# Kernel tuning notes

Measured on AMD Instinct MI355X. Metric: run time of the kernel, lower is better.

The kernel has to match this reference:

```python
import jax, jax.numpy as jnp
import numpy as np

N, E, G = 50000, 800000, 64
IN, ED = 2, 2
H1, C1 = 16, 8
H2, C2 = 4, 16
D1 = H1 * C1  # 128
D2 = H2 * C2  # 64


def _glorot(key, shape):
    fan_in, fan_out = shape[0], shape[-1]
    lim = jnp.sqrt(6.0 / (fan_in + fan_out))
    return jax.random.uniform(key, shape, jnp.float32, -lim, lim)


def setup_inputs() -> dict:
    key = jax.random.key(0)
    ks = jax.random.split(key, 16)
    x = jax.random.normal(ks[0], (N, IN), jnp.float32)
    edge_attr = jax.random.uniform(ks[1], (E, ED), jnp.float32)
    edge_index = jax.random.randint(ks[2], (2, E), 0, N, jnp.int64)
    batch = jnp.sort(jax.random.randint(ks[3], (N,), 0, G, jnp.int64))
    return {
        'x': x, 'edge_attr': edge_attr,
        'W_l1': _glorot(ks[4], (IN, D1)), 'b_l1': jnp.zeros((D1,), jnp.float32),
        'W_r1': _glorot(ks[5], (IN, D1)), 'b_r1': jnp.zeros((D1,), jnp.float32),
        'W_e1': _glorot(ks[6], (ED, D1)),
        'att1': _glorot(ks[7], (H1, C1)),
        'bias1': jnp.zeros((D1,), jnp.float32),
        'W_l2': _glorot(ks[8], (D1, D2)), 'b_l2': jnp.zeros((D2,), jnp.float32),
        'W_r2': _glorot(ks[9], (D1, D2)), 'b_r2': jnp.zeros((D2,), jnp.float32),
        'W_e2': _glorot(ks[10], (ED, D2)),
        'att2': _glorot(ks[11], (H2, C2)),
        'bias2': jnp.zeros((D2,), jnp.float32),
        'edge_index': edge_index, 'batch': batch,
    }


def _gatv2(x, edge_attr, src, tgt, Wl, bl, Wr, br, We, att, bias, H, C):
    n = x.shape[0]
    xl = (x @ Wl + bl).reshape(n, H, C)          # source transform (lin_l)
    xr = (x @ Wr + br).reshape(n, H, C)          # target transform (lin_r)
    xe = (edge_attr @ We).reshape(-1, H, C)      # edge transform (no bias)
    m = xl[src] + xr[tgt] + xe                   # [E,H,C]
    e = jnp.einsum('ehc,hc->eh', jax.nn.leaky_relu(m, 0.2), att)  # [E,H]
    emax = jax.ops.segment_max(e, tgt, num_segments=n)
    ee = jnp.exp(e - emax[tgt])
    denom = jax.ops.segment_sum(ee, tgt, num_segments=n)
    alpha = ee / denom[tgt]                      # segment softmax over in-edges
    out = jax.ops.segment_sum(alpha[:, :, None] * xl[src], tgt, num_segments=n)
    return out.reshape(n, H * C) + bias


def reference(x, edge_attr, W_l1, b_l1, W_r1, b_r1, W_e1, att1, bias1,
              W_l2, b_l2, W_r2, b_r2, W_e2, att2, bias2, edge_index, batch):
    src, tgt = edge_index[0], edge_index[1]
    h = _gatv2(x, edge_attr, src, tgt, W_l1, b_l1, W_r1, b_r1, W_e1, att1, bias1, H1, C1)
    h = jax.nn.elu(h)  # dropout is identity in eval mode
    h = _gatv2(h, edge_attr, src, tgt, W_l2, b_l2, W_r2, b_r2, W_e2, att2, bias2, H2, C2)
    # global_mean_pool over graphs
    sums = jax.ops.segment_sum(h, batch, num_segments=G)
    cnts = jax.ops.segment_sum(jnp.ones((h.shape[0], 1), h.dtype), batch, num_segments=G)
    return sums / jnp.maximum(cnts, 1.0)
```

## Files before the change

### kernel.cpp

```cpp
#include <hip/hip_runtime.h>
#include <math.h>

#define NBLK 256


template<int CTRL>
__device__ __forceinline__ float dppf(float x) {
    return __int_as_float(__builtin_amdgcn_update_dpp(
        0, __float_as_int(x), CTRL, 0xF, 0xF, true));
}
__device__ __forceinline__ float quadsum(float x) {
    x += dppf<0xB1>(x);
    x += dppf<0x4E>(x);
    return x;
}
__device__ __forceinline__ float sum16(float x) {
    x += dppf<0xB1>(x);
    x += dppf<0x4E>(x);
    x += dppf<0x141>(x);
    x += dppf<0x140>(x);
    return x;
}


__global__ __launch_bounds__(256) void k_hist(const int* __restrict__ tgt,
                                              int* __restrict__ gh,
                                              int e, int chunk, int nbuck) {
    __shared__ int lh[256];
    int tid = threadIdx.x, blk = blockIdx.x;
    lh[tid] = 0;
    __syncthreads();
    int lo = blk * chunk, hi = min(lo + chunk, e);
    for (int i = lo + tid; i < hi; i += 256)
        atomicAdd(&lh[tgt[i] >> 8], 1);
    __syncthreads();
    if (tid < nbuck) gh[tid * NBLK + blk] = lh[tid];
}


__global__ __launch_bounds__(256) void k_scanA(const int* __restrict__ deg,
                                               int* __restrict__ excl,
                                               int* __restrict__ bsum, int n) {
    int i = blockIdx.x * 256 + threadIdx.x;
    int lane = threadIdx.x & 63, wv = threadIdx.x >> 6;
    int v = (i < n) ? deg[i] : 0;
    int incl = v;
#pragma unroll
    for (int off = 1; off < 64; off <<= 1) {
        int t = __shfl_up(incl, off);
        if (lane >= off) incl += t;
    }
    __shared__ int ws[4];
    if (lane == 63) ws[wv] = incl;
    __syncthreads();
    int prefix = 0;
    for (int k = 0; k < wv; ++k) prefix += ws[k];
    if (i < n) excl[i] = prefix + incl - v;
    if (threadIdx.x == 255) bsum[blockIdx.x] = prefix + incl;
}

__global__ __launch_bounds__(256) void k_scanB(const int* __restrict__ bsum, int* __restrict__ boff,
                                               int* __restrict__ total_at, int nb, int n) {
    __shared__ int ws[4];
    __shared__ int carry_s;
    int lane = threadIdx.x & 63, wv = threadIdx.x >> 6;
    if (threadIdx.x == 0) carry_s = 0;
    __syncthreads();
    for (int base = 0; base < nb; base += 256) {
        int i = base + threadIdx.x;
        int v = (i < nb) ? bsum[i] : 0;
        int incl = v;
#pragma unroll
        for (int off = 1; off < 64; off <<= 1) {
            int t = __shfl_up(incl, off);
            if (lane >= off) incl += t;
        }
        if (lane == 63) ws[wv] = incl;
        __syncthreads();
        int prefix = carry_s;
        for (int k = 0; k < wv; ++k) prefix += ws[k];
        if (i < nb) boff[i] = prefix + incl - v;
        __syncthreads();
        if (threadIdx.x == 255) carry_s = prefix + incl;
        __syncthreads();
    }
    if (threadIdx.x == 0) total_at[n] = carry_s;
}

__global__ void k_scanC(int* __restrict__ arr, const int* __restrict__ boff, int n) {
    int i = blockIdx.x * 256 + threadIdx.x;
    if (i < n) arr[i] += boff[blockIdx.x];
}


__global__ __launch_bounds__(256) void k_binplace(const int* __restrict__ src,
                                                  const int* __restrict__ tgt,
                                                  const float* __restrict__ ea,
                                                  const float* __restrict__ x,
                                                  const int* __restrict__ gexcl,
                                                  float4* __restrict__ brec,
                                                  int* __restrict__ bmeta,
                                                  int e, int chunk, int nbuck) {
    __shared__ int loff[256];
    int tid = threadIdx.x, blk = blockIdx.x;
    if (tid < nbuck) loff[tid] = gexcl[tid * NBLK + blk];
    __syncthreads();
    int lo = blk * chunk, hi = min(lo + chunk, e);
    for (int i = lo + tid; i < hi; i += 256) {
        int t = tgt[i], s = src[i];
        float2 ev = ((const float2*)ea)[i];
        float2 xv = *(const float2*)(x + 2 * (size_t)s);
        int dst = atomicAdd(&loff[t >> 8], 1);
        brec[dst] = make_float4(xv.x, xv.y, ev.x, ev.y);
        bmeta[dst] = (s & 0xFFFF) | ((t & 0xFF) << 16);
    }
}


__global__ __launch_bounds__(256) void k_place2(const int* __restrict__ gexcl,
                                                const int* __restrict__ bmeta,
                                                const float4* __restrict__ brec,
                                                float4* __restrict__ col_rec,
                                                int* __restrict__ col_src,
                                                int* __restrict__ rowp, int n) {
    __shared__ int hist[256];
    __shared__ int pos[256];
    __shared__ int ws[4];
    int b = blockIdx.x, tid = threadIdx.x;
    int lo = gexcl[b * NBLK], hi = gexcl[(b + 1) * NBLK];
    hist[tid] = 0;
    __syncthreads();
    for (int i = lo + tid; i < hi; i += 256)
        atomicAdd(&hist[(bmeta[i] >> 16) & 0xFF], 1);
    __syncthreads();
    int lane = tid & 63, wv = tid >> 6;
    int v = hist[tid];
    int incl = v;
#pragma unroll
    for (int off = 1; off < 64; off <<= 1) {
        int t = __shfl_up(incl, off);
        if (lane >= off) incl += t;
    }
    if (lane == 63) ws[wv] = incl;
    __syncthreads();
    int prefix = 0;
    for (int k = 0; k < wv; ++k) prefix += ws[k];
    int rp = lo + prefix + incl - v;
    int node = b * 256 + tid;
    if (node <= n) rowp[node] = rp;
    if (b == (int)gridDim.x - 1 && tid == 0) rowp[n] = hi;
    pos[tid] = rp;
    __syncthreads();
    for (int i = lo + tid; i < hi; i += 256) {
        int m = bmeta[i];
        float4 r = brec[i];
        int slot = atomicAdd(&pos[(m >> 16) & 0xFF], 1);
        col_rec[slot] = r;
        col_src[slot] = m & 0xFFFF;
    }
}


__global__ __launch_bounds__(256) void k_agg1(
    const float* __restrict__ x,
    const int* __restrict__ rowp,
    const float4* __restrict__ col_rec,
    const float* __restrict__ W_l1, const float* __restrict__ b_l1,
    const float* __restrict__ W_r1, const float* __restrict__ b_r1,
    const float* __restrict__ W_e1,
    const float* __restrict__ att1,
    const float* __restrict__ bias1,
    float* __restrict__ hpost,
    int n)
{
    int wid = (blockIdx.x * blockDim.x + threadIdx.x) >> 6;
    if (wid >= n) return;
    int v = __builtin_amdgcn_readfirstlane(wid);
    int lane = threadIdx.x & 63;
    int f0 = 2 * lane, f1 = 2 * lane + 1;

    float Wl00 = W_l1[f0], Wl10 = W_l1[128 + f0], bl0 = b_l1[f0];
    float Wl01 = W_l1[f1], Wl11 = W_l1[128 + f1], bl1 = b_l1[f1];
    float We00 = W_e1[f0], We10 = W_e1[128 + f0];
    float We01 = W_e1[f1], We11 = W_e1[128 + f1];
    float a0 = att1[f0], a1 = att1[f1];

    float xv0 = x[2 * v], xv1 = x[2 * v + 1];
    float xrA = xv0 * W_r1[f0] + xv1 * W_r1[128 + f0] + b_r1[f0];
    float xrB = xv0 * W_r1[f1] + xv1 * W_r1[128 + f1] + b_r1[f1];

    float lh = 0.f, acc0 = 0.f, acc1 = 0.f;
    int rs = rowp[v], re = rowp[v + 1];
    bool b0 = (lane & 1) != 0, b1 = (lane & 2) != 0;

    int cs = rs;
#define E1(K, R) \
    float xa##K = fmaf(R.x, Wl00, fmaf(R.y, Wl10, bl0)); \
    float xb##K = fmaf(R.x, Wl01, fmaf(R.y, Wl11, bl1)); \
    float s##K; { \
        float m0 = xa##K + xrA + R.z * We00 + R.w * We10; \
        float m1 = xb##K + xrB + R.z * We01 + R.w * We11; \
        s##K = quadsum(fmaf(fmaxf(m0, 0.2f * m0), a0, fmaxf(m1, 0.2f * m1) * a1)); \
    }
    for (; cs + 4 <= re; cs += 4) {
        float4 r0 = col_rec[cs + 0];
        float4 r1 = col_rec[cs + 1];
        float4 r2 = col_rec[cs + 2];
        float4 r3 = col_rec[cs + 3];
        E1(0, r0) E1(1, r1) E1(2, r2) E1(3, r3)
        float sel01 = b0 ? s1 : s0;
        float sel23 = b0 ? s3 : s2;
        float smy = b1 ? sel23 : sel01;
        float p = __expf(smy);
        float p0 = dppf<0x00>(p), p1 = dppf<0x55>(p), p2 = dppf<0xAA>(p), p3 = dppf<0xFF>(p);
        lh += (p0 + p1) + (p2 + p3);
        acc0 += fmaf(p0, xa0, p1 * xa1) + fmaf(p2, xa2, p3 * xa3);
        acc1 += fmaf(p0, xb0, p1 * xb1) + fmaf(p2, xb2, p3 * xb3);
    }
#undef E1
    for (; cs < re; ++cs) {
        float4 r = col_rec[cs];
        float xa = fmaf(r.x, Wl00, fmaf(r.y, Wl10, bl0));
        float xb = fmaf(r.x, Wl01, fmaf(r.y, Wl11, bl1));
        float m0 = xa + xrA + r.z * We00 + r.w * We10;
        float m1 = xb + xrB + r.z * We01 + r.w * We11;
        float s = quadsum(fmaf(fmaxf(m0, 0.2f * m0), a0, fmaxf(m1, 0.2f * m1) * a1));
        float p = __expf(s);
        lh += p;
        acc0 = fmaf(p, xa, acc0);
        acc1 = fmaf(p, xb, acc1);
    }

    float r0o, r1o;
    if (re > rs) { float inv = 1.f / lh; r0o = acc0 * inv; r1o = acc1 * inv; }
    else { r0o = 0.f; r1o = 0.f; }
    r0o += bias1[f0]; r1o += bias1[f1];
    r0o = (r0o > 0.f) ? r0o : (__expf(r0o) - 1.f);
    r1o = (r1o > 0.f) ? r1o : (__expf(r1o) - 1.f);
    *(float2*)(hpost + (size_t)v * 128 + f0) = make_float2(r0o, r1o);
}


struct XF2Shared {
    float4 hs[64 * 32];
    float4 ws[128 * 16];
};

__device__ __forceinline__ void xf2_pass(XF2Shared& sm,
                                         const float* __restrict__ W,
                                         const float* __restrict__ b,
                                         float* __restrict__ out,
                                         int v0, int n, int t) {
    __syncthreads();
    {
        const float4* wsrc = (const float4*)W;
#pragma unroll
        for (int i = 0; i < 8; ++i) sm.ws[t + 256 * i] = wsrc[t + 256 * i];
    }
    __syncthreads();

    int lane = t & 63, w = t >> 6;
    int fg = lane & 3, ng = lane >> 2;
    int fq = 4 * w + fg;
    int hsw = ng & 7;

    float acc[4][4];
#pragma unroll
    for (int i = 0; i < 4; ++i)
#pragma unroll
        for (int c = 0; c < 4; ++c) acc[i][c] = 0.f;

    for (int kq = 0; kq < 32; ++kq) {
        float4 w0 = sm.ws[(4 * kq + 0) * 16 + fq];
        float4 w1 = sm.ws[(4 * kq + 1) * 16 + fq];
        float4 w2 = sm.ws[(4 * kq + 2) * 16 + fq];
        float4 w3 = sm.ws[(4 * kq + 3) * 16 + fq];
        int ks = kq ^ hsw;
        float4 h0 = sm.hs[(4 * ng + 0) * 32 + ks];
        float4 h1 = sm.hs[(4 * ng + 1) * 32 + ks];
        float4 h2 = sm.hs[(4 * ng + 2) * 32 + ks];
        float4 h3 = sm.hs[(4 * ng + 3) * 32 + ks];
#pragma unroll
        for (int i = 0; i < 4; ++i) {
            float4 h = (i == 0) ? h0 : (i == 1) ? h1 : (i == 2) ? h2 : h3;
            acc[i][0] += h.x * w0.x; acc[i][1] += h.x * w0.y; acc[i][2] += h.x * w0.z; acc[i][3] += h.x * w0.w;
            acc[i][0] += h.y * w1.x; acc[i][1] += h.y * w1.y; acc[i][2] += h.y * w1.z; acc[i][3] += h.y * w1.w;
            acc[i][0] += h.z * w2.x; acc[i][1] += h.z * w2.y; acc[i][2] += h.z * w2.z; acc[i][3] += h.z * w2.w;
            acc[i][0] += h.w * w3.x; acc[i][1] += h.w * w3.y; acc[i][2] += h.w * w3.z; acc[i][3] += h.w * w3.w;
        }
    }

    float4 bf = ((const float4*)b)[fq];
#pragma unroll
    for (int i = 0; i < 4; ++i) {
        int node = v0 + 4 * ng + i;
        if (node < n) {
            float4 r = make_float4(acc[i][0] + bf.x, acc[i][1] + bf.y,
                                   acc[i][2] + bf.z, acc[i][3] + bf.w);
            *(float4*)(out + (size_t)node * 64 + 4 * fq) = r;
        }
    }
}

__global__ __launch_bounds__(256) void k_transform2(
    const float* __restrict__ hpost,
    const float* __restrict__ W_l2, const float* __restrict__ b_l2,
    const float* __restrict__ W_r2, const float* __restrict__ b_r2,
    float* __restrict__ xl2, float* __restrict__ xr2, int n)
{
    __shared__ XF2Shared sm;
    int t = threadIdx.x;
    int v0 = blockIdx.x * 64;
    {
        int node = t >> 2, sub = t & 3;
        int sw = (node >> 2) & 7;
        bool valid = (v0 + node) < n;
        const float4* src = (const float4*)(hpost + (size_t)(v0 + node) * 128);
#pragma unroll
        for (int i = 0; i < 8; ++i) {
            int kq = sub + 4 * i;
            float4 val = valid ? src[kq] : make_float4(0.f, 0.f, 0.f, 0.f);
            sm.hs[node * 32 + (kq ^ sw)] = val;
        }
    }
    xf2_pass(sm, W_l2, b_l2, xl2, v0, n, t);
    xf2_pass(sm, W_r2, b_r2, xr2, v0, n, t);
}


__global__ __launch_bounds__(256) void k_agg2(
    const float* __restrict__ xl2,
    const float* __restrict__ xr2,
    const int* __restrict__ rowp,
    const int* __restrict__ col_src,
    const float4* __restrict__ col_rec,
    const float* __restrict__ W_e2,
    const float* __restrict__ att2,
    const float* __restrict__ bias2,
    float* __restrict__ h2,
    int n)
{
    int wid = (blockIdx.x * blockDim.x + threadIdx.x) >> 6;
    if (wid >= n) return;
    int v = __builtin_amdgcn_readfirstlane(wid);
    int lane = threadIdx.x & 63;
    float We0 = W_e2[lane], We1 = W_e2[64 + lane];
    float a = att2[lane];
    float xr = xr2[(size_t)v * 64 + lane];
    float lh = 0.f, acc = 0.f;
    int rs = rowp[v], re = rowp[v + 1];
    const float2* eap = (const float2*)col_rec;
    bool b0 = (lane & 1) != 0, b1 = (lane & 2) != 0;

    int cs = rs;
#define E2(K, EV, XL) \
    float s##K; { \
        float m = XL + xr + EV.x * We0 + EV.y * We1; \
        s##K = sum16(fmaxf(m, 0.2f * m) * a); \
    }
    for (; cs + 4 <= re; cs += 4) {
        int u0 = col_src[cs], u1 = col_src[cs + 1], u2 = col_src[cs + 2], u3 = col_src[cs + 3];
        float2 e0 = eap[2 * cs + 1], e1 = eap[2 * cs + 3];
        float2 e2 = eap[2 * cs + 5], e3 = eap[2 * cs + 7];
        float xl0 = xl2[(size_t)u0 * 64 + lane];
        float xl1 = xl2[(size_t)u1 * 64 + lane];
        float xl2_ = xl2[(size_t)u2 * 64 + lane];
        float xl3 = xl2[(size_t)u3 * 64 + lane];
        E2(0, e0, xl0) E2(1, e1, xl1) E2(2, e2, xl2_) E2(3, e3, xl3)
        float sel01 = b0 ? s1 : s0;
        float sel23 = b0 ? s3 : s2;
        float smy = b1 ? sel23 : sel01;
        float p = __expf(smy);
        float p0 = dppf<0x00>(p), p1 = dppf<0x55>(p), p2 = dppf<0xAA>(p), p3 = dppf<0xFF>(p);
        lh += (p0 + p1) + (p2 + p3);
        acc += fmaf(p0, xl0, p1 * xl1) + fmaf(p2, xl2_, p3 * xl3);
    }
#undef E2
    for (; cs < re; ++cs) {
        int u = col_src[cs];
        float2 ev = eap[2 * cs + 1];
        float xl = xl2[(size_t)u * 64 + lane];
        float m = xl + xr + ev.x * We0 + ev.y * We1;
        float s = sum16(fmaxf(m, 0.2f * m) * a);
        float p = __expf(s);
        lh += p;
        acc = fmaf(p, xl, acc);
    }
    float r = (re > rs) ? acc / lh : 0.f;
    h2[(size_t)v * 64 + lane] = r + bias2[lane];
}


__global__ __launch_bounds__(256) void k_pool2(const float* __restrict__ h2,
                                               const int* __restrict__ batch,
                                               float* __restrict__ sums, float* __restrict__ cnt,
                                               int n, int chunk) {
    int w = (blockIdx.x * blockDim.x + threadIdx.x) >> 6;
    int lane = threadIdx.x & 63;
    int start = w * chunk;
    if (start >= n) return;
    int end = min(n, start + chunk);
    int g = batch[start];
    float acc = 0.f;
    int c = 0;
    for (int v = start; v < end; ++v) {
        int bg = batch[v];
        if (bg != g) {
            atomicAdd(&sums[g * 64 + lane], acc);
            if (lane == 0) atomicAdd(&cnt[g], (float)c);
            acc = 0.f; c = 0; g = bg;
        }
        acc += h2[(size_t)v * 64 + lane];
        ++c;
    }
    atomicAdd(&sums[g * 64 + lane], acc);
    if (lane == 0) atomicAdd(&cnt[g], (float)c);
}

__global__ void k_final(const float* __restrict__ sums, const float* __restrict__ cnt,
                        float* __restrict__ out, int g) {
    int i = blockIdx.x * blockDim.x + threadIdx.x;
    if (i < g * 64) out[i] = sums[i] / fmaxf(cnt[i >> 6], 1.f);
}


extern "C" void kernel_launch(void* const* d_in, const int* in_sizes, int n_in,
                              void* d_out, int out_size, void* d_ws, size_t ws_size,
                              hipStream_t stream) {
    const float* x     = (const float*)d_in[0];
    const float* ea    = (const float*)d_in[1];
    const float* W_l1  = (const float*)d_in[2];
    const float* b_l1  = (const float*)d_in[3];
    const float* W_r1  = (const float*)d_in[4];
    const float* b_r1  = (const float*)d_in[5];
    const float* W_e1  = (const float*)d_in[6];
    const float* att1  = (const float*)d_in[7];
    const float* bias1 = (const float*)d_in[8];
    const float* W_l2  = (const float*)d_in[9];
    const float* b_l2  = (const float*)d_in[10];
    const float* W_r2  = (const float*)d_in[11];
    const float* b_r2  = (const float*)d_in[12];
    const float* W_e2  = (const float*)d_in[13];
    const float* att2  = (const float*)d_in[14];
    const float* bias2 = (const float*)d_in[15];
    const int* eidx    = (const int*)d_in[16];
    const int* batch   = (const int*)d_in[17];

    int n = in_sizes[0] / 2;
    int e = in_sizes[16] / 2;
    int g = out_size / 64;
    const int* srcI = eidx;
    const int* tgtI = eidx + e;
    int nb = (n + 255) / 256;
    int ntot = nb * NBLK;
    int nb2 = (ntot + 255) / 256;
    int chunk = (e + NBLK - 1) / NBLK;

    char* w = (char*)d_ws;
    size_t off = 0;
    auto take = [&](size_t bytes) -> char* {
        size_t a = (off + 255) & ~(size_t)255;
        off = a + bytes;
        return w + a;
    };
    char*   reg1    = take((size_t)n * 128 * 4);
    float4* brec    = (float4*)reg1;
    float*  hpost   = (float*)reg1;
    float*  h2      = hpost;
    char*   reg2    = take((size_t)n * 64 * 4);
    int*    bmeta   = (int*)reg2;
    float*  xl2     = (float*)reg2;

    float*  xr2     = (float*)take((size_t)n * 64 * 4);
    float4* col_rec = (float4*)take((size_t)e * 16);
    int*    col_src = (int*)take((size_t)e * 4);
    int*    rowp    = (int*)take((size_t)(n + 1) * 4);
    int*    gh      = (int*)take((size_t)ntot * 4);
    int*    gexcl   = (int*)take((size_t)(ntot + 1) * 4);
    int*    gbsum   = (int*)take((size_t)nb2 * 4);
    int*    gboff   = (int*)take((size_t)nb2 * 4);
    float*  sums    = (float*)take((size_t)g * 64 * 4);
    float*  cnt     = (float*)take((size_t)g * 4);

    hipMemsetAsync(sums, 0, (size_t)g * 64 * 4, stream);
    hipMemsetAsync(cnt, 0, (size_t)g * 4, stream);

    k_hist<<<NBLK, 256, 0, stream>>>(tgtI, gh, e, chunk, nb);
    k_scanA<<<nb2, 256, 0, stream>>>(gh, gexcl, gbsum, ntot);
    k_scanB<<<1, 256, 0, stream>>>(gbsum, gboff, gexcl, nb2, ntot);
    k_scanC<<<nb2, 256, 0, stream>>>(gexcl, gboff, ntot);
    k_binplace<<<NBLK, 256, 0, stream>>>(srcI, tgtI, ea, x, gexcl, brec, bmeta, e, chunk, nb);
    k_place2<<<nb, 256, 0, stream>>>(gexcl, bmeta, brec, col_rec, col_src, rowp, n);

    int nwaveblocks = (n * 64 + 255) / 256;
    k_agg1<<<nwaveblocks, 256, 0, stream>>>(x, rowp, col_rec,
                                            W_l1, b_l1, W_r1, b_r1, W_e1, att1, bias1,
                                            hpost, n);
    int ntiles = (n + 63) / 64;
    k_transform2<<<ntiles, 256, 0, stream>>>(hpost, W_l2, b_l2, W_r2, b_r2, xl2, xr2, n);
    k_agg2<<<nwaveblocks, 256, 0, stream>>>(xl2, xr2, rowp, col_src, col_rec,
                                            W_e2, att2, bias2, h2, n);

    int pool_waves = 1024;
    int pool_chunk = (n + pool_waves - 1) / pool_waves;
    k_pool2<<<pool_waves / 4, 256, 0, stream>>>(h2, batch, sums, cnt, n, pool_chunk);
    k_final<<<(g * 64 + 255) / 256, 256, 0, stream>>>(sums, cnt, (float*)d_out, g);
}
```

Before: 186.7 us.

## Fold scan fixup into consumers, replace memsets with one init kernel, double NBLK

Removes the k_scanC pass by having k_binplace and k_place2 add the per-256 block offset themselves when reading the global exclusive scan, and computes the upper bound for the last bucket from e. The two hipMemsetAsync calls become a single tiny init kernel. NBLK doubles to 512, so the histogram and binplace passes use more blocks and smaller chunks, at the cost of a larger scan array. The aim is fewer launches and less serialized work in the CSR build.

```diff
diff --git a/kernel.cpp b/kernel.cpp
--- a/kernel.cpp
+++ b/kernel.cpp
@@ -1,7 +1,7 @@
 #include <hip/hip_runtime.h>
 #include <math.h>
 
-#define NBLK 256
+#define NBLK 512
 
 
 template<int CTRL>
@@ -20,6 +20,13 @@
     x += dppf<0x141>(x);
     x += dppf<0x140>(x);
     return x;
+}
+
+
+__global__ void k_init(float* __restrict__ sums, float* __restrict__ cnt, int gn) {
+    int i = blockIdx.x * 256 + threadIdx.x;
+    if (i < gn * 64) sums[i] = 0.f;
+    if (i < gn) cnt[i] = 0.f;
 }
 
 
@@ -60,7 +67,7 @@
 }
 
 __global__ __launch_bounds__(256) void k_scanB(const int* __restrict__ bsum, int* __restrict__ boff,
-                                               int* __restrict__ total_at, int nb, int n) {
+                                               int nb) {
     __shared__ int ws[4];
     __shared__ int carry_s;
     int lane = threadIdx.x & 63, wv = threadIdx.x >> 6;
@@ -84,12 +91,6 @@
         if (threadIdx.x == 255) carry_s = prefix + incl;
         __syncthreads();
     }
-    if (threadIdx.x == 0) total_at[n] = carry_s;
-}
-
-__global__ void k_scanC(int* __restrict__ arr, const int* __restrict__ boff, int n) {
-    int i = blockIdx.x * 256 + threadIdx.x;
-    if (i < n) arr[i] += boff[blockIdx.x];
 }
 
 
@@ -98,12 +99,16 @@
                                                   const float* __restrict__ ea,
                                                   const float* __restrict__ x,
                                                   const int* __restrict__ gexcl,
+                                                  const int* __restrict__ gboff,
                                                   float4* __restrict__ brec,
                                                   int* __restrict__ bmeta,
                                                   int e, int chunk, int nbuck) {
     __shared__ int loff[256];
     int tid = threadIdx.x, blk = blockIdx.x;
-    if (tid < nbuck) loff[tid] = gexcl[tid * NBLK + blk];
+    if (tid < nbuck) {
+        int cell = tid * NBLK + blk;
+        loff[tid] = gexcl[cell] + gboff[cell >> 8];
+    }
     __syncthreads();
     int lo = blk * chunk, hi = min(lo + chunk, e);
     for (int i = lo + tid; i < hi; i += 256) {
@@ -118,16 +123,20 @@
 
 
 __global__ __launch_bounds__(256) void k_place2(const int* __restrict__ gexcl,
+                                                const int* __restrict__ gboff,
                                                 const int* __restrict__ bmeta,
                                                 const float4* __restrict__ brec,
                                                 float4* __restrict__ col_rec,
                                                 int* __restrict__ col_src,
-                                                int* __restrict__ rowp, int n) {
+                                                int* __restrict__ rowp,
+                                                int n, int ntot, int e) {
     __shared__ int hist[256];
     __shared__ int pos[256];
     __shared__ int ws[4];
     int b = blockIdx.x, tid = threadIdx.x;
-    int lo = gexcl[b * NBLK], hi = gexcl[(b + 1) * NBLK];
+    int clo = b * NBLK, chi = clo + NBLK;
+    int lo = gexcl[clo] + gboff[clo >> 8];
+    int hi = (chi >= ntot) ? e : (gexcl[chi] + gboff[chi >> 8]);
     hist[tid] = 0;
     __syncthreads();
     for (int i = lo + tid; i < hi; i += 256)
@@ -482,15 +491,15 @@
     float*  sums    = (float*)take((size_t)g * 64 * 4);
     float*  cnt     = (float*)take((size_t)g * 4);
 
-    hipMemsetAsync(sums, 0, (size_t)g * 64 * 4, stream);
-    hipMemsetAsync(cnt, 0, (size_t)g * 4, stream);
+    k_init<<<(g * 64 + 255) / 256, 256, 0, stream>>>(sums, cnt, g);
 
     k_hist<<<NBLK, 256, 0, stream>>>(tgtI, gh, e, chunk, nb);
     k_scanA<<<nb2, 256, 0, stream>>>(gh, gexcl, gbsum, ntot);
-    k_scanB<<<1, 256, 0, stream>>>(gbsum, gboff, gexcl, nb2, ntot);
-    k_scanC<<<nb2, 256, 0, stream>>>(gexcl, gboff, ntot);
-    k_binplace<<<NBLK, 256, 0, stream>>>(srcI, tgtI, ea, x, gexcl, brec, bmeta, e, chunk, nb);
-    k_place2<<<nb, 256, 0, stream>>>(gexcl, bmeta, brec, col_rec, col_src, rowp, n);
+    k_scanB<<<1, 256, 0, stream>>>(gbsum, gboff, nb2);
+    k_binplace<<<NBLK, 256, 0, stream>>>(srcI, tgtI, ea, x, gexcl, gboff, brec, bmeta,
+                                         e, chunk, nb);
+    k_place2<<<nb, 256, 0, stream>>>(gexcl, gboff, bmeta, brec, col_rec, col_src, rowp,
+                                     n, ntot, e);
 
     int nwaveblocks = (n * 64 + 255) / 256;
     k_agg1<<<nwaveblocks, 256, 0, stream>>>(x, rowp, col_rec,
```

Result: no change. 185.1 us (-0.8%).
